# Kernel optimization log

Hardware: AMD Instinct MI355X
Metric: run time of the kernel (lower is better)

Reference implementation:

```python
import jax, jax.numpy as jnp
import numpy as np

V, E, HD, T = 32000, 100, 256, 17   # vocab, embed dim, lstm hidden (bidir total), tagset
B, S = 64, 1024
H = HD // 2                         # per-direction hidden


def setup_inputs() -> dict:
    key = jax.random.key(0)
    ks = jax.random.split(key, 16)
    p = lambda k, sh: (jax.random.normal(k, sh, jnp.float32) * 0.1)
    sentence = jax.random.randint(ks[0], (B, S), 0, V)
    mask = jnp.ones((B, S), dtype=bool)
    embed = p(ks[1], (V, E)).at[0].set(0.0)  # padding_idx=0
    inp = {
        "sentence": sentence,
        "mask": mask,
        "embed": embed,
        "w_ih_f": p(ks[2], (4 * H, E)), "w_hh_f": p(ks[3], (4 * H, H)),
        "b_ih_f": p(ks[4], (4 * H,)), "b_hh_f": p(ks[5], (4 * H,)),
        "w_ih_b": p(ks[6], (4 * H, E)), "w_hh_b": p(ks[7], (4 * H, H)),
        "b_ih_b": p(ks[8], (4 * H,)), "b_hh_b": p(ks[9], (4 * H,)),
        "fc_w": p(ks[10], (T, HD)), "fc_b": p(ks[11], (T,)),
        "start_trans": p(ks[12], (T,)),
        "end_trans": p(ks[13], (T,)),
        "trans": p(ks[14], (T, T)),
    }
    return inp


def _lstm_dir(xs, w_ih, w_hh, b_ih, b_hh):
    # xs: [S, B, E] -> hs: [S, B, H]. PyTorch gate order: i, f, g, o.
    xg = jnp.einsum('sbe,ge->sbg', xs, w_ih) + b_ih  # precompute input projections
    h0 = jnp.zeros((xs.shape[1], H), xs.dtype)
    def step(carry, xg_t):
        h, c = carry
        g = xg_t + h @ w_hh.T + b_hh
        i, f, gg, o = jnp.split(g, 4, axis=-1)
        c = jax.nn.sigmoid(f) * c + jax.nn.sigmoid(i) * jnp.tanh(gg)
        h = jax.nn.sigmoid(o) * jnp.tanh(c)
        return (h, c), h
    _, hs = jax.lax.scan(step, (h0, h0), xg)
    return hs


def _emissions(sentence, embed, w_ih_f, w_hh_f, b_ih_f, b_hh_f,
               w_ih_b, w_hh_b, b_ih_b, b_hh_b, fc_w, fc_b):
    x = embed[sentence]                      # [B, S, E] (dropout is identity in eval)
    xs = x.transpose(1, 0, 2)                # [S, B, E]
    hf = _lstm_dir(xs, w_ih_f, w_hh_f, b_ih_f, b_hh_f)
    hb = _lstm_dir(xs[::-1], w_ih_b, w_hh_b, b_ih_b, b_hh_b)[::-1]
    hcat = jnp.concatenate([hf, hb], axis=-1)            # [S, B, 2H]
    return jnp.einsum('sbh,th->sbt', hcat, fc_w) + fc_b  # [S, B, T]


def reference(sentence, mask, embed, w_ih_f, w_hh_f, b_ih_f, b_hh_f,
              w_ih_b, w_hh_b, b_ih_b, b_hh_b, fc_w, fc_b,
              start_trans, end_trans, trans):
    em = _emissions(sentence, embed, w_ih_f, w_hh_f, b_ih_f, b_hh_f,
                    w_ih_b, w_hh_b, b_ih_b, b_hh_b, fc_w, fc_b)  # [S, B, T]
    mk = mask.T  # [S, B]

    # Viterbi forward pass (max-plus recurrence over the tagset)
    score0 = start_trans + em[0]  # [B, T]
    def vstep(score, inp):
        emit_t, mask_t = inp
        ns = score[:, :, None] + trans[None] + emit_t[:, None, :]  # [B, T_prev, T_cur]
        best = ns.max(axis=1)
        idx = jnp.argmax(ns, axis=1)                                # [B, T]
        score = jnp.where(mask_t[:, None], best, score)
        return score, idx
    score, hist = jax.lax.scan(vstep, score0, (em[1:], mk[1:]))    # hist: [S-1, B, T]
    score = score + end_trans
    last_tag = jnp.argmax(score, axis=-1)                          # [B]

    # Backtrace (mask-aware: frozen past sequence end)
    def back(tag, inp):
        idx_t, mask_t = inp
        prev = jnp.take_along_axis(idx_t, tag[:, None], axis=1)[:, 0]
        tag = jnp.where(mask_t, prev, tag)
        return tag, tag
    _, ys = jax.lax.scan(back, last_tag, (hist, mk[1:]), reverse=True)  # [S-1, B]
    path = jnp.concatenate([ys, last_tag[None]], axis=0).T              # [B, S]
    return path
```

## Files before the change

### kernel.cpp

```cpp
#include <hip/hip_runtime.h>
#include <math.h>

#define S_LEN 1024
#define BATCH 64
#define EDIM  100
#define HDIM  128
#define G4    512
#define TAGS  17
#define SGRP  15

typedef __attribute__((ext_vector_type(2))) float f32x2;
typedef __attribute__((ext_vector_type(4))) float f32x4;

__device__ __forceinline__ f32x2 pkfma(f32x2 a, f32x2 b, f32x2 c) {
    return __builtin_elementwise_fma(a, b, c);
}

template<int CTRL>
__device__ __forceinline__ float qperm(float x) {
    int i = __float_as_int(x);
    i = __builtin_amdgcn_update_dpp(0, i, CTRL, 0xF, 0xF, true);
    return __int_as_float(i);
}
#define QX1 qperm<0xB1>
#define QX2 qperm<0x4E>

__device__ __forceinline__ float fast_tanh_u(float x) {
    float e = __expf(-2.f * x);
    return fmaf(2.f, __builtin_amdgcn_rcpf(1.f + e), -1.f);
}

#define RDLANE(v, jj) __int_as_float(__builtin_amdgcn_readlane(__float_as_int(v), (jj)))

#define STEP_BARRIER() do {                                          \
    __builtin_amdgcn_sched_barrier(0);                               \
    asm volatile("s_waitcnt lgkmcnt(0)\n\ts_barrier" ::: "memory");  \
    __builtin_amdgcn_sched_barrier(0);                               \
} while (0)

__global__ __launch_bounds__(512, 1) void fused_scan_proj(
    const float* __restrict__ xgf_s, const float* __restrict__ xgb_s,
    const float* __restrict__ w_hh_f, const float* __restrict__ w_hh_b,
    float* __restrict__ hcat, float* __restrict__ h_state, float* __restrict__ c_state,
    int t0_scan, int clen, int nscan,
    const int* __restrict__ sentence, const float* __restrict__ embed,
    const float* __restrict__ w_ih_f, const float* __restrict__ b_ih_f, const float* __restrict__ b_hh_f,
    const float* __restrict__ w_ih_b, const float* __restrict__ b_ih_b, const float* __restrict__ b_hh_b,
    float* __restrict__ xgf_p, float* __restrict__ xgb_p, int t0_proj)
{
    __shared__ __align__(16) float smem[3232];

    if ((int)blockIdx.x < nscan) {
        const int t     = threadIdx.x;
        const int gid   = t >> 2, q = t & 3;
        const int b     = blockIdx.x & 63;
        const int dir   = blockIdx.x >> 6;
        const int chain = blockIdx.x;

        const float* whh = dir ? w_hh_b : w_hh_f;
        f32x2 wl[4][8], wh[4][8];
#pragma unroll
        for (int g4 = 0; g4 < 4; ++g4) {
            const f32x4* wr = (const f32x4*)(whh + (g4 * HDIM + gid) * HDIM + q * 32);
#pragma unroll
            for (int i = 0; i < 8; ++i) {
                f32x4 v = wr[i];
                wl[g4][i] = v.xy;
                wh[g4][i] = v.zw;
            }
        }

        typedef float hl_t[4][36];
        hl_t* h_lds = (hl_t*)smem;
        float c_reg = 0.f;
        if (t0_scan == 0) {
            if (t < HDIM) h_lds[0][t >> 5][t & 31] = 0.f;
        } else {
            c_reg = c_state[chain * HDIM + gid];
            if (t < HDIM) h_lds[0][t >> 5][t & 31] = h_state[chain * HDIM + t];
        }
        __syncthreads();

        const float* xgp = (dir ? xgb_s : xgf_s) + (long)b * G4 + gid * 4;
        float4 z4; z4.x = z4.y = z4.z = z4.w = 0.f;
        float4 xgc = *(const float4*)xgp;
        float4 xgn = (clen > 1) ? *(const float4*)(xgp + (long)BATCH * G4) : z4;

        float* hc_base = hcat + (long)b * S_LEN * 256 + dir * HDIM + gid;
        float hv = 0.f;
        float hbuf[8];

        for (int sb = 0; sb < clen; sb += 8) {
#pragma unroll
            for (int k = 0; k < 8; ++k) {
                const int s = sb + k;
                float4 xg2 = z4;
                if (s + 2 < clen) xg2 = *(const float4*)(xgp + (long)(s + 2) * BATCH * G4);

                const int cur = k & 1;
                const float* hp = &h_lds[cur][q][0];
                f32x2 ac0 = {0.f, 0.f}, ac1 = {0.f, 0.f}, ac2 = {0.f, 0.f}, ac3 = {0.f, 0.f};
#pragma unroll
                for (int i = 0; i < 8; ++i) {
                    f32x4 h4 = *(const f32x4*)(hp + i * 4);
                    f32x2 hlo = h4.xy, hhi = h4.zw;
                    ac0 = pkfma(wl[0][i], hlo, ac0); ac0 = pkfma(wh[0][i], hhi, ac0);
                    ac1 = pkfma(wl[1][i], hlo, ac1); ac1 = pkfma(wh[1][i], hhi, ac1);
                    ac2 = pkfma(wl[2][i], hlo, ac2); ac2 = pkfma(wh[2][i], hhi, ac2);
                    ac3 = pkfma(wl[3][i], hlo, ac3); ac3 = pkfma(wh[3][i], hhi, ac3);
                }
                float a0 = ac0.x + ac0.y, a1 = ac1.x + ac1.y;
                float a2 = ac2.x + ac2.y, a3 = ac3.x + ac3.y;

                a0 += QX1(a0); a1 += QX1(a1); a2 += QX1(a2); a3 += QX1(a3);
                a0 += QX2(a0); a1 += QX2(a1); a2 += QX2(a2); a3 += QX2(a3);

                float av = (q == 0) ? a0 : (q == 1) ? a1 : (q == 2) ? a2 : a3;
                float xv = (q == 0) ? xgc.x : (q == 1) ? xgc.y : (q == 2) ? xgc.z : xgc.w;
                float pre = xv + av;
                float xin = (q == 2) ? 2.f * pre : pre;
                float e   = __expf(-xin);
                float sgm = __builtin_amdgcn_rcpf(1.f + e);
                float act = (q == 2) ? fmaf(2.f, sgm, -1.f) : sgm;
                float t1 = QX1(act);
                float t2 = QX2(act);
                float t3 = QX2(t1);
                float gi = (q == 0) ? act : (q == 1) ? t1 : (q == 2) ? t2 : t3;
                float gf = (q == 1) ? act : (q == 0) ? t1 : (q == 3) ? t2 : t3;
                float gg = (q == 2) ? act : (q == 3) ? t1 : (q == 0) ? t2 : t3;
                float go = (q == 3) ? act : (q == 2) ? t1 : (q == 1) ? t2 : t3;
                c_reg = gf * c_reg + gi * gg;
                hv = go * fast_tanh_u(c_reg);
                hbuf[k] = hv;

                if (q == 0) h_lds[cur ^ 1][gid >> 5][gid & 31] = hv;
                STEP_BARRIER();
                xgc = xgn; xgn = xg2;
            }
            if (q == 0) {
#pragma unroll
                for (int k = 0; k < 8; ++k) {
                    int tg = dir ? (S_LEN - 1 - (t0_scan + sb + k)) : (t0_scan + sb + k);
                    hc_base[(long)tg * 256] = hbuf[k];
                }
            }
        }

        if (q == 0) {
            c_state[chain * HDIM + gid] = c_reg;
            h_state[chain * HDIM + gid] = hv;
        }
    } else {
        if (t0_proj < 0) return;
        const int pb   = blockIdx.x - nscan;
        const int tid  = threadIdx.x;
        const int row0 = pb * 16;

        float (*xf)[EDIM] = (float(*)[EDIM])smem;
        float (*xb)[EDIM] = (float(*)[EDIM])(smem + 1600);
        int* tok = (int*)(smem + 3200);

        if (tid < 32) {
            int r = tid & 15;
            int row = row0 + r;
            int s = row >> 6, b = row & 63;
            int tt = (tid < 16) ? (t0_proj + s) : (S_LEN - 1 - (t0_proj + s));
            tok[tid] = sentence[b * S_LEN + tt];
        }
        __syncthreads();
        for (int i = tid; i < 16 * EDIM; i += 512) {
            int r = i / EDIM, e = i - r * EDIM;
            xf[r][e] = embed[(long)tok[r] * EDIM + e];
            xb[r][e] = embed[(long)tok[16 + r] * EDIM + e];
        }
        __syncthreads();

        const float* wptr[2];
        float bias[2];
#pragma unroll
        for (int ci = 0; ci < 2; ++ci) {
            int c = tid + 512 * ci;
            if (c < G4) { wptr[ci] = w_ih_f + c * EDIM; bias[ci] = b_ih_f[c] + b_hh_f[c]; }
            else { int cb = c - G4; wptr[ci] = w_ih_b + cb * EDIM; bias[ci] = b_ih_b[cb] + b_hh_b[cb]; }
        }

        float acc[2][16];
#pragma unroll
        for (int ci = 0; ci < 2; ++ci)
#pragma unroll
            for (int r = 0; r < 16; ++r) acc[ci][r] = 0.f;

        for (int e = 0; e < EDIM; e += 4) {
            float4 w4[2];
#pragma unroll
            for (int ci = 0; ci < 2; ++ci) w4[ci] = *(const float4*)(wptr[ci] + e);
#pragma unroll
            for (int r = 0; r < 16; ++r) {
                float4 xvf = *(const float4*)&xf[r][e];
                float4 xvb = *(const float4*)&xb[r][e];
#pragma unroll
                for (int ci = 0; ci < 2; ++ci) {
                    float4 xv = (ci == 0) ? xvf : xvb;
                    acc[ci][r] = fmaf(w4[ci].x, xv.x, acc[ci][r]);
                    acc[ci][r] = fmaf(w4[ci].y, xv.y, acc[ci][r]);
                    acc[ci][r] = fmaf(w4[ci].z, xv.z, acc[ci][r]);
                    acc[ci][r] = fmaf(w4[ci].w, xv.w, acc[ci][r]);
                }
            }
        }

#pragma unroll
        for (int ci = 0; ci < 2; ++ci) {
            int c = tid + 512 * ci;
#pragma unroll
            for (int r = 0; r < 16; ++r) {
                int row = row0 + r;
                float v = acc[ci][r] + bias[ci];
                if (c < G4) xgf_p[(long)row * G4 + (c & 127) * 4 + (c >> 7)] = v;
                else { int cb = c - G4; xgb_p[(long)row * G4 + (cb & 127) * 4 + (cb >> 7)] = v; }
            }
        }
    }
}

__global__ __launch_bounds__(256) void fc_kernel(
    const float* __restrict__ hcat, const float* __restrict__ fc_w,
    const float* __restrict__ fc_b, float* __restrict__ em)
{
    __shared__ float w_lds[TAGS * 256];
    __shared__ float part[64 * TAGS * 4];
    const int tid = threadIdx.x;
    for (int i = tid; i < TAGS * 256; i += 256) w_lds[i] = fc_w[i];
    __syncthreads();

    const int r = tid >> 2, p = tid & 3;
    const long row = (long)blockIdx.x * 64 + r;
    const float* hrow = hcat + row * 256 + p * 64;

    float acc[TAGS];
#pragma unroll
    for (int tg = 0; tg < TAGS; ++tg) acc[tg] = 0.f;

    for (int e4 = 0; e4 < 16; ++e4) {
        float4 xv = *(const float4*)(hrow + e4 * 4);
        const float* wp = w_lds + p * 64 + e4 * 4;
#pragma unroll
        for (int tg = 0; tg < TAGS; ++tg) {
            acc[tg] = fmaf(xv.x, wp[tg * 256 + 0], acc[tg]);
            acc[tg] = fmaf(xv.y, wp[tg * 256 + 1], acc[tg]);
            acc[tg] = fmaf(xv.z, wp[tg * 256 + 2], acc[tg]);
            acc[tg] = fmaf(xv.w, wp[tg * 256 + 3], acc[tg]);
        }
    }
#pragma unroll
    for (int tg = 0; tg < TAGS; ++tg) part[(r * TAGS + tg) * 4 + p] = acc[tg];
    __syncthreads();

    for (int idx = tid; idx < 64 * TAGS; idx += 256) {
        int rr = idx / TAGS, tg = idx - rr * TAGS;
        const float* pp = part + (rr * TAGS + tg) * 4;
        float v = ((pp[0] + pp[1]) + (pp[2] + pp[3])) + fc_b[tg];
        em[((long)blockIdx.x * 64 + rr) * TAGS + tg] = v;
    }
}

#define MAX3(a,b,c) fmaxf(fmaxf((a),(b)),(c))
#define MIN3(a,b,c) min(min((a),(b)),(c))

__device__ __forceinline__ float max17(const float* a) {
    float m0 = MAX3(a[0], a[1], a[2]);
    float m1 = MAX3(a[3], a[4], a[5]);
    float m2 = MAX3(a[6], a[7], a[8]);
    float m3 = MAX3(a[9], a[10], a[11]);
    float m4 = MAX3(a[12], a[13], a[14]);
    float m5 = fmaxf(a[15], a[16]);
    float n0 = MAX3(m0, m1, m2);
    float n1 = MAX3(m3, m4, m5);
    return fmaxf(n0, n1);
}

__global__ __launch_bounds__(64) void viterbi_score(
    const float* __restrict__ em,
    const float* __restrict__ start_trans, const float* __restrict__ end_trans,
    const float* __restrict__ trans,
    float* __restrict__ scores, int* __restrict__ last_tag)
{
    const int b = blockIdx.x;
    const int lane = threadIdx.x;
    __shared__ __align__(16) float e_lds[S_LEN * TAGS];

    {
        const float4* ef4 = (const float4*)(em + (long)b * S_LEN * TAGS);
        float4* el4 = (float4*)e_lds;
        for (int i = lane; i < (S_LEN * TAGS) / 4; i += 64) el4[i] = ef4[i];
    }
    const int cl = (lane < TAGS) ? lane : 0;
    float tcol[TAGS], etr[TAGS];
#pragma unroll
    for (int jj = 0; jj < TAGS; ++jj) {
        tcol[jj] = trans[jj * TAGS + cl];
        etr[jj]  = end_trans[jj];
    }
    __syncthreads();

    float sc = start_trans[cl] + e_lds[cl];
    float* sb = scores + (long)b * S_LEN * TAGS + cl;
    if (lane < TAGS) sb[0] = sc;

    float em_cur = e_lds[1 * TAGS + cl];
#pragma unroll 2
    for (int s = 1; s < S_LEN; ++s) {
        int sn = (s + 1 < S_LEN) ? (s + 1) : s;
        float em_next = e_lds[sn * TAGS + cl];

        float a[TAGS];
#pragma unroll
        for (int jj = 0; jj < TAGS; ++jj)
            a[jj] = RDLANE(sc, jj) + tcol[jj];

        float amax = max17(a);
        sc = amax + em_cur;
        if (lane < TAGS) sb[(long)s * TAGS] = sc;
        em_cur = em_next;
    }

    {
        float ev[TAGS];
#pragma unroll
        for (int jj = 0; jj < TAGS; ++jj) ev[jj] = RDLANE(sc, jj) + etr[jj];
        float bestv = max17(ev);
        int c[17];
#pragma unroll
        for (int j = 0; j < 17; ++j) c[j] = (ev[j] == bestv) ? j : 255;
        int m0 = MIN3(c[0], c[1], c[2]);
        int m1 = MIN3(c[3], c[4], c[5]);
        int m2 = MIN3(c[6], c[7], c[8]);
        int m3 = MIN3(c[9], c[10], c[11]);
        int m4 = MIN3(c[12], c[13], c[14]);
        int m5 = min(c[15], c[16]);
        int bt = min(MIN3(m0, m1, m2), MIN3(m3, m4, m5));
        if (lane == 0) last_tag[b] = bt;
    }
}

__global__ __launch_bounds__(256) void hist_kernel(
    const float* __restrict__ scores, const float* __restrict__ em,
    const float* __restrict__ trans, unsigned char* __restrict__ hist_g)
{
    const int nb = (S_LEN - 1 + SGRP - 1) / SGRP;
    const int b = blockIdx.x / nb, g = blockIdx.x % nb;
    const int t = threadIdx.x;
    __shared__ float s_sc[(SGRP + 1) * TAGS];
    __shared__ float s_em[(SGRP + 1) * TAGS];
    __shared__ float s_tr[TAGS * TAGS];

    const long b_base = (long)b * S_LEN * TAGS;
    const long maxoff = (long)S_LEN * TAGS - 1;
    for (int i = t; i < (SGRP + 1) * TAGS; i += 256) {
        long off = (long)g * SGRP * TAGS + i;
        long co  = off > maxoff ? maxoff : off;
        s_sc[i] = scores[b_base + co];
        s_em[i] = em[b_base + co];
    }
    for (int i = t; i < TAGS * TAGS; i += 256) s_tr[i] = trans[i];
    __syncthreads();

    if (t >= SGRP * TAGS) return;
    const int sl = t / TAGS, c = t - sl * TAGS;
    const int s = g * SGRP + sl + 1;
    if (s >= S_LEN) return;

    const float* sprev = s_sc + sl * TAGS;
    const float emv = s_em[(sl + 1) * TAGS + c];
    const float cur = s_sc[(sl + 1) * TAGS + c];

    int bi = 255;
#pragma unroll
    for (int j = TAGS - 1; j >= 0; --j) {
        float v = (sprev[j] + s_tr[j * TAGS + c]) + emv;
        if (v == cur) bi = j;
    }
    hist_g[((long)b * S_LEN + s) * TAGS + c] = (unsigned char)bi;
}

__global__ __launch_bounds__(64) void backtrace_kernel(
    const unsigned char* __restrict__ hist_g, const int* __restrict__ last_tag,
    int* __restrict__ out)
{
    const int b = blockIdx.x;
    const int lane = threadIdx.x;
    __shared__ int hist_i[(S_LEN * TAGS) / 4];
    __shared__ int tags[S_LEN];

    const int* hg = (const int*)(hist_g + (long)b * S_LEN * TAGS);
    for (int i = lane; i < (S_LEN * TAGS) / 4; i += 64) hist_i[i] = hg[i];
    __syncthreads();

    if (lane == 0) {
        const unsigned char* hl = (const unsigned char*)hist_i;
        int tag = last_tag[b];
        tags[S_LEN - 1] = tag;
        for (int s = S_LEN - 2; s >= 0; --s) {
            tag = hl[(s + 1) * TAGS + tag];
            tags[s] = tag;
        }
    }
    __syncthreads();
    for (int t = lane; t < S_LEN; t += 64) out[b * S_LEN + t] = tags[t];
}

extern "C" void kernel_launch(void* const* d_in, const int* in_sizes, int n_in,
                              void* d_out, int out_size, void* d_ws, size_t ws_size,
                              hipStream_t stream) {
    const int*   sentence    = (const int*)d_in[0];
    const float* embed       = (const float*)d_in[2];
    const float* w_ih_f      = (const float*)d_in[3];
    const float* w_hh_f      = (const float*)d_in[4];
    const float* b_ih_f      = (const float*)d_in[5];
    const float* b_hh_f      = (const float*)d_in[6];
    const float* w_ih_b      = (const float*)d_in[7];
    const float* w_hh_b      = (const float*)d_in[8];
    const float* b_ih_b      = (const float*)d_in[9];
    const float* b_hh_b      = (const float*)d_in[10];
    const float* fc_w        = (const float*)d_in[11];
    const float* fc_b        = (const float*)d_in[12];
    const float* start_trans = (const float*)d_in[13];
    const float* end_trans   = (const float*)d_in[14];
    const float* trans       = (const float*)d_in[15];
    int* out = (int*)d_out;

    const size_t hcat_e = (size_t)S_LEN * BATCH * 256;
    const size_t em_e   = (size_t)S_LEN * BATCH * TAGS;
    const size_t st_e   = (size_t)128 * HDIM;
    const size_t hist_e = (em_e + 3) / 4;
    const size_t fixed  = hcat_e + 2 * em_e + 2 * st_e + hist_e + 64;
    static const int cands[] = {1024, 512, 256, 128, 64};
    int C = 64;
    for (int ci = 0; ci < 5; ++ci) {
        int nch = S_LEN / cands[ci];
        size_t nbuf = (nch == 1) ? 2 : 4;
        size_t need = (nbuf * (size_t)cands[ci] * BATCH * G4 + fixed) * 4;
        if (need <= ws_size) { C = cands[ci]; break; }
    }
    const int nchunk = S_LEN / C;
    const size_t xg1 = (size_t)C * BATCH * G4;

    float* ws   = (float*)d_ws;
    float* xgf0 = ws;
    float* xgb0 = xgf0 + xg1;
    float* xgf1 = xgb0 + xg1;
    float* xgb1 = (nchunk > 1) ? xgf1 + xg1 : xgb0;
    float* base = (nchunk > 1) ? xgb1 + xg1 : xgf1;
    float* hcat     = base;
    float* em       = hcat + hcat_e;
    float* h_state  = em + em_e;
    float* c_state  = h_state + st_e;
    float* scores   = c_state + st_e;
    unsigned char* hist_g = (unsigned char*)(scores + em_e);
    int*   last_tag = (int*)(scores + em_e + hist_e);

    const int nproj = C * 4;

    fused_scan_proj<<<nproj, 512, 0, stream>>>(
        nullptr, nullptr, w_hh_f, w_hh_b, hcat, h_state, c_state, 0, 0, 0,
        sentence, embed, w_ih_f, b_ih_f, b_hh_f, w_ih_b, b_ih_b, b_hh_b,
        xgf0, xgb0, 0);

    for (int k = 0; k < nchunk; ++k) {
        const bool par1 = (k & 1) != 0;
        float* sf = par1 ? xgf1 : xgf0;
        float* sbx = par1 ? xgb1 : xgb0;
        float* pf = par1 ? xgf0 : xgf1;
        float* pbx = par1 ? xgb0 : xgb1;
        const bool hp = (k + 1 < nchunk);
        const int grid = 128 + (hp ? nproj : 0);
        fused_scan_proj<<<grid, 512, 0, stream>>>(
            sf, sbx, w_hh_f, w_hh_b, hcat, h_state, c_state, k * C, C, 128,
            sentence, embed, w_ih_f, b_ih_f, b_hh_f, w_ih_b, b_ih_b, b_hh_b,
            pf, pbx, hp ? (k + 1) * C : -1);
    }

    fc_kernel<<<(S_LEN * BATCH) / 64, 256, 0, stream>>>(hcat, fc_w, fc_b, em);
    viterbi_score<<<BATCH, 64, 0, stream>>>(
        em, start_trans, end_trans, trans, scores, last_tag);
    const int nb = (S_LEN - 1 + SGRP - 1) / SGRP;
    hist_kernel<<<BATCH * nb, 256, 0, stream>>>(scores, em, trans, hist_g);
    backtrace_kernel<<<BATCH, 64, 0, stream>>>(hist_g, last_tag, out);
}
```

Measured before the change: 1.095 ms.

## Overlap FC emission projection with LSTM scan chunks in fused kernel

Removes the standalone fc_kernel and computes emissions for time chunks whose forward and backward hidden states are both complete, using extra blocks inside the chunked scan/projection launches. A final launch handles the remaining chunks. The aim is to hide FC work behind the latency-bound recurrent scan and save a separate full pass. In exchange, shared memory becomes dynamic and larger on launches that include FC blocks, and the chunk-pairing index logic adds complexity.

```diff
diff --git a/kernel.cpp b/kernel.cpp
--- a/kernel.cpp
+++ b/kernel.cpp
@@ -46,9 +46,11 @@
     const int* __restrict__ sentence, const float* __restrict__ embed,
     const float* __restrict__ w_ih_f, const float* __restrict__ b_ih_f, const float* __restrict__ b_hh_f,
     const float* __restrict__ w_ih_b, const float* __restrict__ b_ih_b, const float* __restrict__ b_hh_b,
-    float* __restrict__ xgf_p, float* __restrict__ xgb_p, int t0_proj)
+    float* __restrict__ xgf_p, float* __restrict__ xgb_p, int t0_proj, int nproj_n,
+    const float* __restrict__ fc_w, const float* __restrict__ fc_b,
+    float* __restrict__ em, int fc_t0a, int fc_t0b)
 {
-    __shared__ __align__(16) float smem[3232];
+    extern __shared__ float smem[];
 
     if ((int)blockIdx.x < nscan) {
         const int t     = threadIdx.x;
@@ -150,7 +152,7 @@
             c_state[chain * HDIM + gid] = c_reg;
             h_state[chain * HDIM + gid] = hv;
         }
-    } else {
+    } else if ((int)blockIdx.x < nscan + nproj_n) {
         if (t0_proj < 0) return;
         const int pb   = blockIdx.x - nscan;
         const int tid  = threadIdx.x;
@@ -220,47 +222,56 @@
                 else { int cb = c - G4; xgb_p[(long)row * G4 + (cb & 127) * 4 + (cb >> 7)] = v; }
             }
         }
-    }
-}
-
-__global__ __launch_bounds__(256) void fc_kernel(
-    const float* __restrict__ hcat, const float* __restrict__ fc_w,
-    const float* __restrict__ fc_b, float* __restrict__ em)
-{
-    __shared__ float w_lds[TAGS * 256];
-    __shared__ float part[64 * TAGS * 4];
-    const int tid = threadIdx.x;
-    for (int i = tid; i < TAGS * 256; i += 256) w_lds[i] = fc_w[i];
-    __syncthreads();
-
-    const int r = tid >> 2, p = tid & 3;
-    const long row = (long)blockIdx.x * 64 + r;
-    const float* hrow = hcat + row * 256 + p * 64;
-
-    float acc[TAGS];
-#pragma unroll
-    for (int tg = 0; tg < TAGS; ++tg) acc[tg] = 0.f;
-
-    for (int e4 = 0; e4 < 16; ++e4) {
-        float4 xv = *(const float4*)(hrow + e4 * 4);
-        const float* wp = w_lds + p * 64 + e4 * 4;
-#pragma unroll
-        for (int tg = 0; tg < TAGS; ++tg) {
-            acc[tg] = fmaf(xv.x, wp[tg * 256 + 0], acc[tg]);
-            acc[tg] = fmaf(xv.y, wp[tg * 256 + 1], acc[tg]);
-            acc[tg] = fmaf(xv.z, wp[tg * 256 + 2], acc[tg]);
-            acc[tg] = fmaf(xv.w, wp[tg * 256 + 3], acc[tg]);
-        }
-    }
-#pragma unroll
-    for (int tg = 0; tg < TAGS; ++tg) part[(r * TAGS + tg) * 4 + p] = acc[tg];
-    __syncthreads();
-
-    for (int idx = tid; idx < 64 * TAGS; idx += 256) {
-        int rr = idx / TAGS, tg = idx - rr * TAGS;
-        const float* pp = part + (rr * TAGS + tg) * 4;
-        float v = ((pp[0] + pp[1]) + (pp[2] + pp[3])) + fc_b[tg];
-        em[((long)blockIdx.x * 64 + rr) * TAGS + tg] = v;
+    } else {
+        const int fcb0 = blockIdx.x - nscan - nproj_n;
+        const int nfc1 = clen >> 1;
+        int fb, ft0;
+        if (fcb0 < nfc1) { fb = fcb0; ft0 = fc_t0a; }
+        else             { fb = fcb0 - nfc1; ft0 = fc_t0b; }
+        if (ft0 < 0) return;
+
+        const int tid = threadIdx.x;
+        float* w_lds = smem;
+        float* part  = smem + TAGS * 256;
+
+        for (int i = tid; i < TAGS * 256; i += 512) w_lds[i] = fc_w[i];
+        __syncthreads();
+
+        const int r = tid >> 2, p = tid & 3;
+        const int idx0 = fb * 128 + r;
+        const int b  = idx0 / clen;
+        const int i0 = idx0 - b * clen;
+        const long row = (long)b * S_LEN + ft0 + i0;
+        const float* hrow = hcat + row * 256 + p * 64;
+
+        float acc[TAGS];
+#pragma unroll
+        for (int tg = 0; tg < TAGS; ++tg) acc[tg] = 0.f;
+
+        for (int e4 = 0; e4 < 16; ++e4) {
+            float4 xv = *(const float4*)(hrow + e4 * 4);
+            const float* wp = w_lds + p * 64 + e4 * 4;
+#pragma unroll
+            for (int tg = 0; tg < TAGS; ++tg) {
+                acc[tg] = fmaf(xv.x, wp[tg * 256 + 0], acc[tg]);
+                acc[tg] = fmaf(xv.y, wp[tg * 256 + 1], acc[tg]);
+                acc[tg] = fmaf(xv.z, wp[tg * 256 + 2], acc[tg]);
+                acc[tg] = fmaf(xv.w, wp[tg * 256 + 3], acc[tg]);
+            }
+        }
+#pragma unroll
+        for (int tg = 0; tg < TAGS; ++tg) part[(r * TAGS + tg) * 4 + p] = acc[tg];
+        __syncthreads();
+
+        for (int idx = tid; idx < 128 * TAGS; idx += 512) {
+            int rr = idx / TAGS, tg = idx - rr * TAGS;
+            const float* pp = part + (rr * TAGS + tg) * 4;
+            float v = ((pp[0] + pp[1]) + (pp[2] + pp[3])) + fc_b[tg];
+            int ridx = fb * 128 + rr;
+            int bb = ridx / clen;
+            int ii = ridx - bb * clen;
+            em[((long)bb * S_LEN + ft0 + ii) * TAGS + tg] = v;
+        }
     }
 }
 
@@ -460,27 +471,48 @@
     int*   last_tag = (int*)(scores + em_e + hist_e);
 
     const int nproj = C * 4;
-
-    fused_scan_proj<<<nproj, 512, 0, stream>>>(
-        nullptr, nullptr, w_hh_f, w_hh_b, hcat, h_state, c_state, 0, 0, 0,
+    const int nfc1  = C / 2;
+    const size_t SM_SMALL = 3232 * sizeof(float);
+    const size_t SM_FC    = 13056 * sizeof(float);
+
+    fused_scan_proj<<<nproj, 512, SM_SMALL, stream>>>(
+        nullptr, nullptr, w_hh_f, w_hh_b, hcat, h_state, c_state, 0, C, 0,
         sentence, embed, w_ih_f, b_ih_f, b_hh_f, w_ih_b, b_ih_b, b_hh_b,
-        xgf0, xgb0, 0);
+        xgf0, xgb0, 0, nproj, fc_w, fc_b, em, -1, -1);
 
     for (int k = 0; k < nchunk; ++k) {
         const bool par1 = (k & 1) != 0;
-        float* sf = par1 ? xgf1 : xgf0;
+        float* sf  = par1 ? xgf1 : xgf0;
         float* sbx = par1 ? xgb1 : xgb0;
-        float* pf = par1 ? xgf0 : xgf1;
+        float* pf  = par1 ? xgf0 : xgf1;
         float* pbx = par1 ? xgb0 : xgb1;
         const bool hp = (k + 1 < nchunk);
-        const int grid = 128 + (hp ? nproj : 0);
-        fused_scan_proj<<<grid, 512, 0, stream>>>(
+        const int np = hp ? nproj : 0;
+
+        int fca = -1, fcb = -1, nr = 0;
+        if (2 * k >= nchunk + 1) {
+            int m1 = k - 1, m2 = nchunk - k;
+            fca = m1 * C; nr = 1;
+            if (m2 != m1) { fcb = m2 * C; nr = 2; }
+        }
+        const int grid = 128 + np + nr * nfc1;
+        const size_t sm = (nr > 0) ? SM_FC : SM_SMALL;
+        fused_scan_proj<<<grid, 512, sm, stream>>>(
             sf, sbx, w_hh_f, w_hh_b, hcat, h_state, c_state, k * C, C, 128,
             sentence, embed, w_ih_f, b_ih_f, b_hh_f, w_ih_b, b_ih_b, b_hh_b,
-            pf, pbx, hp ? (k + 1) * C : -1);
-    }
-
-    fc_kernel<<<(S_LEN * BATCH) / 64, 256, 0, stream>>>(hcat, fc_w, fc_b, em);
+            pf, pbx, hp ? (k + 1) * C : -1, np,
+            fc_w, fc_b, em, fca, fcb);
+    }
+    {
+        int fca = (nchunk - 1) * C;
+        int fcb = (nchunk > 1) ? 0 : -1;
+        int nr  = (nchunk > 1) ? 2 : 1;
+        fused_scan_proj<<<nr * nfc1, 512, SM_FC, stream>>>(
+            nullptr, nullptr, w_hh_f, w_hh_b, hcat, h_state, c_state, 0, C, 0,
+            sentence, embed, w_ih_f, b_ih_f, b_hh_f, w_ih_b, b_ih_b, b_hh_b,
+            nullptr, nullptr, -1, 0, fc_w, fc_b, em, fca, fcb);
+    }
+
     viterbi_score<<<BATCH, 64, 0, stream>>>(
         em, start_trans, end_trans, trans, scores, last_tag);
     const int nb = (S_LEN - 1 + SGRP - 1) / SGRP;
```

New measurement: 1.088 ms. No clear change (-0.6%).
